# Kernel tuning notes

Hardware: AMD Instinct MI355X
Metric: run time of the kernel (lower is better)

Reference implementation:

```python
import jax, jax.numpy as jnp
import numpy as np

D_MODEL = 1024
HEADS = 16
DEPTH = D_MODEL // HEADS
B, S = 4, 4096
EPS_K = 1e-6  # kernel feature epsilon
EPS_LN = 1e-6


def setup_inputs() -> dict:
    key = jax.random.key(0)
    ks = jax.random.split(key, 8)
    lecun = 1.0 / np.sqrt(D_MODEL)  # LecunNormal stddev
    glorot = np.sqrt(2.0 / (D_MODEL + D_MODEL))  # keras Dense default
    return {
        "q": jax.random.normal(ks[0], (B, S, D_MODEL), jnp.float32),
        "k": jax.random.normal(ks[1], (B, S, D_MODEL), jnp.float32),
        "v": jax.random.normal(ks[2], (B, S, D_MODEL), jnp.float32),
        "mask": jnp.ones((B, S), jnp.float32),
        "wq": jax.random.normal(ks[3], (D_MODEL, D_MODEL), jnp.float32) * lecun,
        "wk": jax.random.normal(ks[4], (D_MODEL, D_MODEL), jnp.float32) * lecun,
        "wv": jax.random.normal(ks[5], (D_MODEL, D_MODEL), jnp.float32) * lecun,
        "ln_gamma": jnp.ones((D_MODEL,), jnp.float32),
        "ln_beta": jnp.zeros((D_MODEL,), jnp.float32),
        "dense_w": jax.random.normal(ks[6], (D_MODEL, D_MODEL), jnp.float32) * glorot,
        "dense_b": jnp.zeros((D_MODEL,), jnp.float32),
    }


def _layernorm(x, g, b):
    m = jnp.mean(x, axis=-1, keepdims=True)
    var = jnp.var(x, axis=-1, keepdims=True)
    return (x - m) * jax.lax.rsqrt(var + EPS_LN) * g + b


def _split_heads(x):
    bsz, sl, _ = x.shape
    return x.reshape(bsz, sl, HEADS, DEPTH).transpose(0, 2, 1, 3)  # [B,H,S,depth]


def reference(q, k, v, mask, wq, wk, wv, ln_gamma, ln_beta, dense_w, dense_b):
    bsz = q.shape[0]
    em = mask[:, None, :, None]  # [B,1,S,1] broadcast over heads/depth
    qh = _split_heads(_layernorm(q @ wq, ln_gamma, ln_beta))
    kh = _split_heads(_layernorm(k @ wk, ln_gamma, ln_beta))
    vh = _split_heads(_layernorm(v @ wv, ln_gamma, ln_beta))
    q_prime = jax.nn.relu(qh) + EPS_K
    k_prime = (jax.nn.relu(kh) + EPS_K) * em
    vh = vh * em
    kv = jnp.einsum('bhnd,bhne->bhde', k_prime, vh)  # [B,H,depth,depth]
    z = 1.0 / (jnp.einsum('bhnd,bhd->bhn', q_prime, k_prime.sum(axis=-2)) + EPS_K)
    att = jnp.einsum('bhnd,bhde,bhn->bhne', q_prime, kv, z)  # [B,H,S,depth]
    # Faithful to original: reshape WITHOUT transposing heads back.
    att = att.reshape(bsz, -1, D_MODEL)  # [B,S,d_model]
    out = att @ dense_w + dense_b
    return _layernorm(out, ln_gamma, ln_beta)
```

## Files before the change

kernel.cpp:

```cpp
#include <hip/hip_runtime.h>
#include <hip/hip_bf16.h>
#include <stdint.h>

#define D_MODEL 1024
#define S_LEN   4096
#define BATCH   4
#define HEADS   16
#define DEPTH   64
#define ROWS    (BATCH*S_LEN)
#define EPS_K_F 1e-6f
#define EPS_LN_F 1e-6f

typedef __attribute__((ext_vector_type(8))) short short8;
typedef __attribute__((ext_vector_type(4))) float f32x4;

__device__ __forceinline__ unsigned short f2bf(float f) {
  union { float f; unsigned u; } x; x.f = f;
  unsigned r = x.u + 0x7FFF + ((x.u >> 16) & 1);
  return (unsigned short)(r >> 16);
}
__device__ __forceinline__ float bf2f(unsigned short b) {
  union { unsigned u; float f; } x; x.u = ((unsigned)b) << 16;
  return x.f;
}
__device__ __forceinline__ void gload16(const void* g, void* l) {
  __builtin_amdgcn_global_load_lds(
      (const __attribute__((address_space(1))) void*)g,
      (__attribute__((address_space(3))) void*)l, 16, 0, 0);
}

__global__ __launch_bounds__(256) void cvt_f32_bf16_k(
    const float* __restrict__ in, unsigned short* __restrict__ out, int n4) {
  int i = blockIdx.x * 256 + threadIdx.x;
  if (i < n4) {
    float4 v = ((const float4*)in)[i];
    ushort4 o;
    o.x = f2bf(v.x); o.y = f2bf(v.y); o.z = f2bf(v.z); o.w = f2bf(v.w);
    ((ushort4*)out)[i] = o;
  }
}

__global__ __launch_bounds__(256) void wtrans_k(
    const float* __restrict__ W, unsigned short* __restrict__ Wt) {
  __shared__ float tile[32][33];
  int n0 = blockIdx.x * 32, k0 = blockIdx.y * 32;
  int tx = threadIdx.x & 31, ty = threadIdx.x >> 5;
  #pragma unroll
  for (int i = 0; i < 32; i += 8)
    tile[ty + i][tx] = W[(size_t)(k0 + ty + i) * D_MODEL + n0 + tx];
  __syncthreads();
  #pragma unroll
  for (int i = 0; i < 32; i += 8)
    Wt[(size_t)(n0 + ty + i) * D_MODEL + k0 + tx] = f2bf(tile[tx][ty + i]);
}

__global__ __launch_bounds__(512, 2) void gemm_bt_k(
    const unsigned short* __restrict__ A,
    const unsigned short* __restrict__ Bt,
    unsigned short* __restrict__ Cb,
    float* __restrict__ psum, float* __restrict__ psq,
    const float* __restrict__ bias,
    int M, int N, int K) {
  __shared__ unsigned short Al[2][256 * 64];
  __shared__ unsigned short Bl[2][256 * 64];
  int t = threadIdx.x;
  int lane = t & 63, wid = t >> 6;
  int wr = wid >> 2, wcn = wid & 3;
  int l15 = lane & 15, lhi = lane >> 4;
  int p = blockIdx.x;
  int cb = (p >> 3) & 3;
  int rb = (p & 7) | ((p >> 5) << 3);
  size_t m0 = (size_t)rb * 256, n0 = (size_t)cb * 256;
  f32x4 acc[8][4] = {};

  const int KT = K >> 6;
  #pragma unroll
  for (int sub = 0; sub < 4; ++sub) {
    int idx = sub * 512 + t;
    int r = idx >> 3, cl = idx & 7;
    int cg = cl ^ (r & 7);
    gload16(A  + (m0 + r) * (size_t)K + cg * 8, &Al[0][idx * 8]);
    gload16(Bt + (n0 + r) * (size_t)K + cg * 8, &Bl[0][idx * 8]);
  }
  asm volatile("s_waitcnt vmcnt(0)" ::: "memory");
  __builtin_amdgcn_s_barrier();
  __builtin_amdgcn_sched_barrier(0);

  for (int kt = 0; kt < KT; ++kt) {
    int cbuf = kt & 1;
    bool pf = (kt + 1) < KT;
    int k0n = (kt + 1) << 6;
    #pragma unroll
    for (int ph = 0; ph < 4; ++ph) {
      const int kk = ph >> 1, mh = ph & 1;
      if (pf && ph == 0) {
        #pragma unroll
        for (int sub = 0; sub < 4; ++sub) {
          int idx = sub * 512 + t;
          int r = idx >> 3, cl = idx & 7;
          int cg = cl ^ (r & 7);
          gload16(A + (m0 + r) * (size_t)K + k0n + cg * 8,
                  &Al[cbuf ^ 1][idx * 8]);
        }
        __builtin_amdgcn_sched_barrier(0);
      }
      if (pf && ph == 1) {
        #pragma unroll
        for (int sub = 0; sub < 4; ++sub) {
          int idx = sub * 512 + t;
          int r = idx >> 3, cl = idx & 7;
          int cg = cl ^ (r & 7);
          gload16(Bt + (n0 + r) * (size_t)K + k0n + cg * 8,
                  &Bl[cbuf ^ 1][idx * 8]);
        }
        __builtin_amdgcn_sched_barrier(0);
      }
      const int cx = (kk * 4 + lhi) ^ (l15 & 7);
      short8 af[4], bfr[4];
      #pragma unroll
      for (int m = 0; m < 4; ++m) {
        int r = wr * 128 + (mh * 4 + m) * 16 + l15;
        af[m] = *(const short8*)&Al[cbuf][r * 64 + cx * 8];
      }
      #pragma unroll
      for (int n = 0; n < 4; ++n) {
        int s = wcn * 64 + n * 16 + l15;
        bfr[n] = *(const short8*)&Bl[cbuf][s * 64 + cx * 8];
      }
      __builtin_amdgcn_s_setprio(1);
      #pragma unroll
      for (int m = 0; m < 4; ++m)
        #pragma unroll
        for (int n = 0; n < 4; ++n)
          acc[mh * 4 + m][n] = __builtin_amdgcn_mfma_f32_16x16x32_bf16(
              af[m], bfr[n], acc[mh * 4 + m][n], 0, 0, 0);
      __builtin_amdgcn_s_setprio(0);
    }
    asm volatile("s_waitcnt vmcnt(0) lgkmcnt(0)" ::: "memory");
    __builtin_amdgcn_s_barrier();
    __builtin_amdgcn_sched_barrier(0);
  }

  if (bias) {
    float bv[4];
    #pragma unroll
    for (int n = 0; n < 4; ++n)
      bv[n] = bias[(int)n0 + wcn * 64 + n * 16 + l15];
    #pragma unroll
    for (int m = 0; m < 8; ++m)
      #pragma unroll
      for (int n = 0; n < 4; ++n)
        #pragma unroll
        for (int j = 0; j < 4; ++j)
          acc[m][n][j] += bv[n];
  }

  int seg = (int)(n0 >> 6) + wcn;
  #pragma unroll
  for (int m = 0; m < 8; ++m) {
    float s[4], s2[4];
    #pragma unroll
    for (int j = 0; j < 4; ++j) {
      float a = 0.f, b = 0.f;
      #pragma unroll
      for (int n = 0; n < 4; ++n) {
        float x = acc[m][n][j];
        a += x; b += x * x;
      }
      s[j] = a; s2[j] = b;
    }
    #pragma unroll
    for (int off = 1; off < 16; off <<= 1) {
      #pragma unroll
      for (int j = 0; j < 4; ++j) {
        s[j]  += __shfl_xor(s[j],  off);
        s2[j] += __shfl_xor(s2[j], off);
      }
    }
    if (l15 == 0) {
      #pragma unroll
      for (int j = 0; j < 4; ++j) {
        int rg = (int)m0 + wr * 128 + m * 16 + lhi * 4 + j;
        psum[rg * 16 + seg] = s[j];
        psq [rg * 16 + seg] = s2[j];
      }
    }
  }

  #pragma unroll
  for (int m = 0; m < 8; ++m)
    #pragma unroll
    for (int j = 0; j < 4; ++j) {
      size_t row = m0 + wr * 128 + m * 16 + lhi * 4 + j;
      #pragma unroll
      for (int n = 0; n < 4; ++n) {
        int col = (int)n0 + wcn * 64 + n * 16 + l15;
        Cb[row * N + col] = f2bf(acc[m][n][j]);
      }
    }
}

__global__ __launch_bounds__(256) void ln_act_k(
    const unsigned short* __restrict__ Cb,
    const float* __restrict__ psum, const float* __restrict__ psq,
    const float* __restrict__ gamma, const float* __restrict__ beta,
    const float* __restrict__ mask,
    unsigned short* __restrict__ out, int mode) {
  int row = blockIdx.x;
  int t = threadIdx.x;
  float s = 0.f, s2 = 0.f;
  #pragma unroll
  for (int i = 0; i < 16; ++i) { s += psum[row * 16 + i]; s2 += psq[row * 16 + i]; }
  float mean = s * (1.f / D_MODEL);
  float var = s2 * (1.f / D_MODEL) - mean * mean;
  float rstd = rsqrtf(var + EPS_LN_F);
  float mk = (mode > 0) ? mask[row] : 1.f;
  ushort4 cv = ((const ushort4*)(Cb + (size_t)row * D_MODEL))[t];
  float4 gv = ((const float4*)gamma)[t];
  float4 bv = ((const float4*)beta)[t];
  float av[4] = {bf2f(cv.x), bf2f(cv.y), bf2f(cv.z), bf2f(cv.w)};
  float g4[4] = {gv.x, gv.y, gv.z, gv.w};
  float b4[4] = {bv.x, bv.y, bv.z, bv.w};
  unsigned short ov[4];
  #pragma unroll
  for (int j = 0; j < 4; ++j) {
    float ln = (av[j] - mean) * rstd * g4[j] + b4[j];
    if (mode == 0)      ln = fmaxf(ln, 0.f) + EPS_K_F;
    else if (mode == 1) ln = (fmaxf(ln, 0.f) + EPS_K_F) * mk;
    else                ln = ln * mk;
    ov[j] = f2bf(ln);
  }
  ushort4 o; o.x = ov[0]; o.y = ov[1]; o.z = ov[2]; o.w = ov[3];
  ((ushort4*)(out + (size_t)row * D_MODEL))[t] = o;
}

__global__ __launch_bounds__(256) void ln_final_k(
    const unsigned short* __restrict__ Cb,
    const float* __restrict__ psum, const float* __restrict__ psq,
    const float* __restrict__ gamma, const float* __restrict__ beta,
    float* __restrict__ out) {
  int row = blockIdx.x;
  int t = threadIdx.x;
  float s = 0.f, s2 = 0.f;
  #pragma unroll
  for (int i = 0; i < 16; ++i) { s += psum[row * 16 + i]; s2 += psq[row * 16 + i]; }
  float mean = s * (1.f / D_MODEL);
  float var = s2 * (1.f / D_MODEL) - mean * mean;
  float rstd = rsqrtf(var + EPS_LN_F);
  ushort4 cv = ((const ushort4*)(Cb + (size_t)row * D_MODEL))[t];
  float4 gv = ((const float4*)gamma)[t];
  float4 bv = ((const float4*)beta)[t];
  float4 w;
  w.x = (bf2f(cv.x) - mean) * rstd * gv.x + bv.x;
  w.y = (bf2f(cv.y) - mean) * rstd * gv.y + bv.y;
  w.z = (bf2f(cv.z) - mean) * rstd * gv.z + bv.z;
  w.w = (bf2f(cv.w) - mean) * rstd * gv.w + bv.w;
  ((float4*)(out + (size_t)row * D_MODEL))[t] = w;
}

__global__ __launch_bounds__(256) void kv_mfma_k(
    const unsigned short* __restrict__ Kp, const unsigned short* __restrict__ Vp,
    float* __restrict__ part, float* __restrict__ kspart) {
  __shared__ unsigned short Kl[4096];
  __shared__ unsigned short Vl[4096];
  int bh = blockIdx.y, chunk = blockIdx.x;
  int b_ = bh >> 4, h = bh & 15;
  int t = threadIdx.x, lane = t & 63, w = t >> 6;
  int l15 = lane & 15, g = lane >> 4;

  int sn = t >> 2, sd16 = t & 3;
  int sc = sd16 ^ ((sn >> 3) & 3);
  size_t goff = (size_t)sn * D_MODEL + h * DEPTH + sd16 * 16;
  int ldst = sn * 64 + sc * 16;

  short8 ones;
  #pragma unroll
  for (int i = 0; i < 8; ++i) ones[i] = (short)0x3F80;

  f32x4 acc[4] = {};
  f32x4 ks = {};

  int baseA = ((w ^ g) << 4) + l15;
  int baseB0 = ((0 ^ g) << 4) + l15;
  int baseB1 = ((1 ^ g) << 4) + l15;
  int baseB2 = ((2 ^ g) << 4) + l15;
  int baseB3 = ((3 ^ g) << 4) + l15;

  size_t rowbase = ((size_t)b_ * S_LEN + (size_t)chunk * 512) * D_MODEL;
  for (int tile = 0; tile < 8; ++tile) {
    const unsigned short* kg = Kp + rowbase + (size_t)tile * 64 * D_MODEL + goff;
    const unsigned short* vg = Vp + rowbase + (size_t)tile * 64 * D_MODEL + goff;
    uint4 ra = *(const uint4*)kg;
    uint4 rb = *(const uint4*)(kg + 8);
    uint4 rc = *(const uint4*)vg;
    uint4 rd = *(const uint4*)(vg + 8);
    __syncthreads();
    *(uint4*)&Kl[ldst]     = ra;
    *(uint4*)&Kl[ldst + 8] = rb;
    *(uint4*)&Vl[ldst]     = rc;
    *(uint4*)&Vl[ldst + 8] = rd;
    __syncthreads();
    #pragma unroll
    for (int kk = 0; kk < 2; ++kk) {
      int nb = (kk * 32 + g * 8) * 64;
      short8 af, bf0, bf1, bf2, bf3;
      #pragma unroll
      for (int i = 0; i < 8; ++i) {
        int rowoff = nb + i * 64;
        af[i]  = (short)Kl[rowoff + baseA];
        bf0[i] = (short)Vl[rowoff + baseB0];
        bf1[i] = (short)Vl[rowoff + baseB1];
        bf2[i] = (short)Vl[rowoff + baseB2];
        bf3[i] = (short)Vl[rowoff + baseB3];
      }
      acc[0] = __builtin_amdgcn_mfma_f32_16x16x32_bf16(af, bf0, acc[0], 0, 0, 0);
      acc[1] = __builtin_amdgcn_mfma_f32_16x16x32_bf16(af, bf1, acc[1], 0, 0, 0);
      acc[2] = __builtin_amdgcn_mfma_f32_16x16x32_bf16(af, bf2, acc[2], 0, 0, 0);
      acc[3] = __builtin_amdgcn_mfma_f32_16x16x32_bf16(af, bf3, acc[3], 0, 0, 0);
      ks     = __builtin_amdgcn_mfma_f32_16x16x32_bf16(af, ones, ks, 0, 0, 0);
    }
  }
  float* pp = part + ((size_t)bh * 8 + chunk) * 4096;
  #pragma unroll
  for (int nf = 0; nf < 4; ++nf)
    #pragma unroll
    for (int r = 0; r < 4; ++r)
      pp[(16 * w + 4 * g + r) * 64 + 16 * nf + l15] = acc[nf][r];
  if (l15 == 0) {
    #pragma unroll
    for (int r = 0; r < 4; ++r)
      kspart[((size_t)bh * 8 + chunk) * 64 + 16 * w + 4 * g + r] = ks[r];
  }
}

__global__ __launch_bounds__(256) void kv_reduce_k(
    const float* __restrict__ part, const float* __restrict__ kspart,
    unsigned short* __restrict__ KVT, float* __restrict__ ksum) {
  int bh = blockIdx.x, t = threadIdx.x;
  for (int idx = t; idx < 4096; idx += 256) {
    int d = idx >> 6, e = idx & 63;
    float s = 0.f;
    #pragma unroll
    for (int c = 0; c < 8; ++c)
      s += part[((size_t)bh * 8 + c) * 4096 + d * 64 + e];
    KVT[(size_t)bh * 4096 + e * 64 + d] = f2bf(s);
  }
  if (t < 64) {
    float s = 0.f;
    #pragma unroll
    for (int c = 0; c < 8; ++c) s += kspart[((size_t)bh * 8 + c) * 64 + t];
    ksum[bh * 64 + t] = s;
  }
}

__global__ __launch_bounds__(256) void att_k(
    const unsigned short* __restrict__ Qp, const unsigned short* __restrict__ KVT,
    const float* __restrict__ ksum, unsigned short* __restrict__ att) {
  __shared__ unsigned short Ql[128 * 64];
  __shared__ unsigned short Kl[64 * 64];
  __shared__ float ksl[64];
  __shared__ float zl[128];
  int bh = blockIdx.y;
  int b = bh >> 4, h = bh & 15;
  int r0 = blockIdx.x * 128;
  int t = threadIdx.x, lane = t & 63, wid = t >> 6;
  int l15 = lane & 15, lhi = lane >> 4;
  #pragma unroll
  for (int i = 0; i < 4; ++i) {
    int cid = i * 256 + t;
    int r = cid >> 3, c8 = cid & 7;
    gload16(Qp + ((size_t)(b * S_LEN + r0 + r)) * D_MODEL + h * DEPTH + c8 * 8,
            &Ql[cid * 8]);
  }
  #pragma unroll
  for (int i = 0; i < 2; ++i) {
    int cid = i * 256 + t;
    gload16(KVT + (size_t)bh * 4096 + cid * 8, &Kl[cid * 8]);
  }
  if (t < 64) ksl[t] = ksum[bh * 64 + t];
  asm volatile("s_waitcnt vmcnt(0)" ::: "memory");
  __syncthreads();
  {
    int r = t >> 1, half = t & 1;
    float s = 0.f;
    #pragma unroll
    for (int j = 0; j < 32; ++j)
      s += bf2f(Ql[r * 64 + half * 32 + j]) * ksl[half * 32 + j];
    s += __shfl_xor(s, 1);
    if (half == 0) zl[r] = 1.f / (s + EPS_K_F);
  }
  __syncthreads();
  f32x4 acc[2][4] = {};
  #pragma unroll
  for (int kk = 0; kk < 2; ++kk) {
    short8 af[2], bfr[4];
    #pragma unroll
    for (int m = 0; m < 2; ++m)
      af[m] = *(const short8*)&Ql[(wid * 32 + m * 16 + l15) * 64 + kk * 32 + lhi * 8];
    #pragma unroll
    for (int n = 0; n < 4; ++n)
      bfr[n] = *(const short8*)&Kl[(n * 16 + l15) * 64 + kk * 32 + lhi * 8];
    #pragma unroll
    for (int m = 0; m < 2; ++m)
      #pragma unroll
      for (int n = 0; n < 4; ++n)
        acc[m][n] = __builtin_amdgcn_mfma_f32_16x16x32_bf16(af[m], bfr[n], acc[m][n], 0, 0, 0);
  }
  #pragma unroll
  for (int m = 0; m < 2; ++m)
    #pragma unroll
    for (int j = 0; j < 4; ++j) {
      int rl = wid * 32 + m * 16 + lhi * 4 + j;
      int n = r0 + rl;
      float z = zl[rl];
      #pragma unroll
      for (int nf = 0; nf < 4; ++nf) {
        int ee = nf * 16 + l15;
        size_t orow = (size_t)b * S_LEN + h * 256 + (n >> 4);
        int ocol = (n & 15) * 64 + ee;
        att[orow * D_MODEL + ocol] = f2bf(acc[m][nf][j] * z);
      }
    }
}

extern "C" void kernel_launch(void* const* d_in, const int* in_sizes, int n_in,
                              void* d_out, int out_size, void* d_ws, size_t ws_size,
                              hipStream_t stream) {
  (void)in_sizes; (void)n_in; (void)out_size; (void)ws_size;
  const float* q     = (const float*)d_in[0];
  const float* k     = (const float*)d_in[1];
  const float* v     = (const float*)d_in[2];
  const float* mask  = (const float*)d_in[3];
  const float* wq    = (const float*)d_in[4];
  const float* wk    = (const float*)d_in[5];
  const float* wv    = (const float*)d_in[6];
  const float* gamma = (const float*)d_in[7];
  const float* beta  = (const float*)d_in[8];
  const float* dw    = (const float*)d_in[9];
  const float* db    = (const float*)d_in[10];
  float* out = (float*)d_out;

  char* ws = (char*)d_ws;
  unsigned short* Xb  = (unsigned short*)(ws);
  unsigned short* Qp  = (unsigned short*)(ws + 33554432);
  unsigned short* Kp  = (unsigned short*)(ws + 67108864);
  unsigned short* Vp  = (unsigned short*)(ws + 100663296);
  unsigned short* WqT = (unsigned short*)(ws + 134217728);
  unsigned short* WkT = WqT + 1048576;
  unsigned short* WvT = WkT + 1048576;
  unsigned short* WdT = WvT + 1048576;
  float* part   = (float*)(ws);
  float* kspart = (float*)(ws + 8388608);
  unsigned short* KVT = (unsigned short*)(ws + 142606336);
  float* ksum = (float*)(ws + 143130624);
  float* psum = (float*)(ws + 143654912);
  float* psq  = (float*)(ws + 144703488);
  unsigned short* Cqkv = (unsigned short*)d_out;
  unsigned short* Cd   = Qp;

  dim3 b256(256);
  dim3 b512(512);
  int n4 = ROWS * D_MODEL / 4;
  dim3 cvtg(n4 / 256);
  dim3 wtg(32, 32);
  dim3 gemmg(256);
  dim3 lng(ROWS);

  wtrans_k<<<wtg, b256, 0, stream>>>(wq, WqT);
  wtrans_k<<<wtg, b256, 0, stream>>>(wk, WkT);
  wtrans_k<<<wtg, b256, 0, stream>>>(wv, WvT);
  wtrans_k<<<wtg, b256, 0, stream>>>(dw, WdT);

  cvt_f32_bf16_k<<<cvtg, b256, 0, stream>>>(q, Xb, n4);
  gemm_bt_k<<<gemmg, b512, 0, stream>>>(Xb, WqT, Cqkv, psum, psq, nullptr, ROWS, D_MODEL, D_MODEL);
  ln_act_k<<<lng, b256, 0, stream>>>(Cqkv, psum, psq, gamma, beta, nullptr, Qp, 0);

  cvt_f32_bf16_k<<<cvtg, b256, 0, stream>>>(k, Xb, n4);
  gemm_bt_k<<<gemmg, b512, 0, stream>>>(Xb, WkT, Cqkv, psum, psq, nullptr, ROWS, D_MODEL, D_MODEL);
  ln_act_k<<<lng, b256, 0, stream>>>(Cqkv, psum, psq, gamma, beta, mask, Kp, 1);

  cvt_f32_bf16_k<<<cvtg, b256, 0, stream>>>(v, Xb, n4);
  gemm_bt_k<<<gemmg, b512, 0, stream>>>(Xb, WvT, Cqkv, psum, psq, nullptr, ROWS, D_MODEL, D_MODEL);
  ln_act_k<<<lng, b256, 0, stream>>>(Cqkv, psum, psq, gamma, beta, mask, Vp, 2);

  kv_mfma_k<<<dim3(8, 64), b256, 0, stream>>>(Kp, Vp, part, kspart);
  kv_reduce_k<<<dim3(64), b256, 0, stream>>>(part, kspart, KVT, ksum);
  att_k<<<dim3(32, 64), b256, 0, stream>>>(Qp, KVT, ksum, Xb);

  gemm_bt_k<<<gemmg, b512, 0, stream>>>(Xb, WdT, Cd, psum, psq, db, ROWS, D_MODEL, D_MODEL);
  ln_final_k<<<lng, b256, 0, stream>>>(Cd, psum, psq, gamma, beta, out);
}
```

Before: 362.0 us.

## Use four-stage K=32 LDS pipeline with partial vmcnt waits in GEMM

Replaces the double-buffered K=64 tile loop with a four-slot ring of K=32 tiles, keeping three tiles of global loads in flight ahead of compute. The full vmcnt(0) wait each iteration becomes a counted partial wait, so the next tile can be consumed while later loads are still outstanding. The LDS swizzle is adapted to 32-wide rows, and B fragments are loaded once per iteration instead of once per phase. The cost is one barrier per 32 K elements instead of per 64, and a fixed-count wait scheme that depends on each tile issuing exactly four loads per thread.

```diff
diff --git a/kernel.cpp b/kernel.cpp
--- a/kernel.cpp
+++ b/kernel.cpp
@@ -61,8 +61,8 @@
     float* __restrict__ psum, float* __restrict__ psq,
     const float* __restrict__ bias,
     int M, int N, int K) {
-  __shared__ unsigned short Al[2][256 * 64];
-  __shared__ unsigned short Bl[2][256 * 64];
+  __shared__ unsigned short Al[4][256 * 32];
+  __shared__ unsigned short Bl[4][256 * 32];
   int t = threadIdx.x;
   int lane = t & 63, wid = t >> 6;
   int wr = wid >> 2, wcn = wid & 3;
@@ -73,60 +73,53 @@
   size_t m0 = (size_t)rb * 256, n0 = (size_t)cb * 256;
   f32x4 acc[8][4] = {};
 
-  const int KT = K >> 6;
-  #pragma unroll
-  for (int sub = 0; sub < 4; ++sub) {
-    int idx = sub * 512 + t;
-    int r = idx >> 3, cl = idx & 7;
-    int cg = cl ^ (r & 7);
-    gload16(A  + (m0 + r) * (size_t)K + cg * 8, &Al[0][idx * 8]);
-    gload16(Bt + (n0 + r) * (size_t)K + cg * 8, &Bl[0][idx * 8]);
-  }
-  asm volatile("s_waitcnt vmcnt(0)" ::: "memory");
+  const int KT = K >> 5;
+
+#define STAGE_TILE(tile_) do {                                              \
+    int kof_ = (tile_) << 5; int slot_ = (tile_) & 3;                       \
+    _Pragma("unroll")                                                       \
+    for (int rnd = 0; rnd < 2; ++rnd) {                                     \
+      int idx = rnd * 512 + t; int r_ = idx >> 2, cl_ = idx & 3;            \
+      int cg_ = cl_ ^ ((r_ >> 1) & 3);                                      \
+      gload16(A + (m0 + r_) * (size_t)K + kof_ + cg_ * 8,                   \
+              &Al[slot_][idx * 8]);                                         \
+    }                                                                       \
+    _Pragma("unroll")                                                       \
+    for (int rnd = 0; rnd < 2; ++rnd) {                                     \
+      int idx = rnd * 512 + t; int r_ = idx >> 2, cl_ = idx & 3;            \
+      int cg_ = cl_ ^ ((r_ >> 1) & 3);                                      \
+      gload16(Bt + (n0 + r_) * (size_t)K + kof_ + cg_ * 8,                  \
+              &Bl[slot_][idx * 8]);                                         \
+    }                                                                       \
+  } while (0)
+
+  STAGE_TILE(0);
+  STAGE_TILE(1);
+  STAGE_TILE(2);
+  asm volatile("s_waitcnt vmcnt(8)" ::: "memory");
   __builtin_amdgcn_s_barrier();
   __builtin_amdgcn_sched_barrier(0);
 
   for (int kt = 0; kt < KT; ++kt) {
-    int cbuf = kt & 1;
-    bool pf = (kt + 1) < KT;
-    int k0n = (kt + 1) << 6;
-    #pragma unroll
-    for (int ph = 0; ph < 4; ++ph) {
-      const int kk = ph >> 1, mh = ph & 1;
-      if (pf && ph == 0) {
-        #pragma unroll
-        for (int sub = 0; sub < 4; ++sub) {
-          int idx = sub * 512 + t;
-          int r = idx >> 3, cl = idx & 7;
-          int cg = cl ^ (r & 7);
-          gload16(A + (m0 + r) * (size_t)K + k0n + cg * 8,
-                  &Al[cbuf ^ 1][idx * 8]);
-        }
-        __builtin_amdgcn_sched_barrier(0);
-      }
-      if (pf && ph == 1) {
-        #pragma unroll
-        for (int sub = 0; sub < 4; ++sub) {
-          int idx = sub * 512 + t;
-          int r = idx >> 3, cl = idx & 7;
-          int cg = cl ^ (r & 7);
-          gload16(Bt + (n0 + r) * (size_t)K + k0n + cg * 8,
-                  &Bl[cbuf ^ 1][idx * 8]);
-        }
-        __builtin_amdgcn_sched_barrier(0);
-      }
-      const int cx = (kk * 4 + lhi) ^ (l15 & 7);
-      short8 af[4], bfr[4];
+    int slot = kt & 3;
+    if (kt + 3 < KT) STAGE_TILE(kt + 3);
+    __builtin_amdgcn_sched_barrier(0);
+    short8 bfr[4];
+    #pragma unroll
+    for (int n = 0; n < 4; ++n) {
+      int rr = wcn * 64 + n * 16 + l15;
+      bfr[n] = *(const short8*)&Bl[slot][rr * 32 + ((lhi ^ ((rr >> 1) & 3)) << 3)];
+    }
+    #pragma unroll
+    for (int mh = 0; mh < 2; ++mh) {
+      short8 af[4];
       #pragma unroll
       for (int m = 0; m < 4; ++m) {
-        int r = wr * 128 + (mh * 4 + m) * 16 + l15;
-        af[m] = *(const short8*)&Al[cbuf][r * 64 + cx * 8];
-      }
-      #pragma unroll
-      for (int n = 0; n < 4; ++n) {
-        int s = wcn * 64 + n * 16 + l15;
-        bfr[n] = *(const short8*)&Bl[cbuf][s * 64 + cx * 8];
-      }
+        int rr = wr * 128 + (mh * 4 + m) * 16 + l15;
+        af[m] = *(const short8*)&Al[slot][rr * 32 + ((lhi ^ ((rr >> 1) & 3)) << 3)];
+      }
+      asm volatile("s_waitcnt lgkmcnt(0)" ::: "memory");
+      __builtin_amdgcn_sched_barrier(0);
       __builtin_amdgcn_s_setprio(1);
       #pragma unroll
       for (int m = 0; m < 4; ++m)
@@ -136,10 +129,18 @@
               af[m], bfr[n], acc[mh * 4 + m][n], 0, 0, 0);
       __builtin_amdgcn_s_setprio(0);
     }
-    asm volatile("s_waitcnt vmcnt(0) lgkmcnt(0)" ::: "memory");
-    __builtin_amdgcn_s_barrier();
-    __builtin_amdgcn_sched_barrier(0);
-  }
+    if (kt + 1 < KT) {
+      if (kt + 4 <= KT - 1)
+        asm volatile("s_waitcnt vmcnt(8)" ::: "memory");
+      else if (kt + 3 == KT - 1)
+        asm volatile("s_waitcnt vmcnt(4)" ::: "memory");
+      else
+        asm volatile("s_waitcnt vmcnt(0)" ::: "memory");
+      __builtin_amdgcn_s_barrier();
+      __builtin_amdgcn_sched_barrier(0);
+    }
+  }
+#undef STAGE_TILE
 
   if (bias) {
     float bv[4];
```

Result: slower. 391.3 us (+8.1%).

## Fuse fp32-to-bf16 input conversion into QKV projection GEMM A-tile loading

Applied to the files above, without the earlier changes.

Removes the three separate cvt_f32_bf16 passes over the q/k/v inputs. A new GEMM variant loads fp32 A tiles into registers, converts them to bf16 and writes them into swizzled LDS, overlapping this with compute on the other buffer. The bf16 intermediate round-trip through memory goes away, but the A loads now use register staging instead of direct global-to-LDS loads and read twice the bytes per tile. The shared compute loop is also restructured: B fragments are loaded once per kk, prefetch is issued all at once, and an explicit lgkmcnt wait comes before the MFMAs.

```diff
diff --git a/kernel.cpp b/kernel.cpp
--- a/kernel.cpp
+++ b/kernel.cpp
@@ -29,17 +29,6 @@
       (__attribute__((address_space(3))) void*)l, 16, 0, 0);
 }
 
-__global__ __launch_bounds__(256) void cvt_f32_bf16_k(
-    const float* __restrict__ in, unsigned short* __restrict__ out, int n4) {
-  int i = blockIdx.x * 256 + threadIdx.x;
-  if (i < n4) {
-    float4 v = ((const float4*)in)[i];
-    ushort4 o;
-    o.x = f2bf(v.x); o.y = f2bf(v.y); o.z = f2bf(v.z); o.w = f2bf(v.w);
-    ((ushort4*)out)[i] = o;
-  }
-}
-
 __global__ __launch_bounds__(256) void wtrans_k(
     const float* __restrict__ W, unsigned short* __restrict__ Wt) {
   __shared__ float tile[32][33];
@@ -52,6 +41,174 @@
   #pragma unroll
   for (int i = 0; i < 32; i += 8)
     Wt[(size_t)(n0 + ty + i) * D_MODEL + k0 + tx] = f2bf(tile[tx][ty + i]);
+}
+
+
+#define GEMM_EPILOGUE(HASBIAS)                                               \
+  if (HASBIAS) {                                                             \
+    float bv[4];                                                             \
+    _Pragma("unroll")                                                        \
+    for (int n = 0; n < 4; ++n)                                              \
+      bv[n] = bias[(int)n0 + wcn * 64 + n * 16 + l15];                       \
+    _Pragma("unroll")                                                        \
+    for (int m = 0; m < 8; ++m)                                              \
+      _Pragma("unroll")                                                      \
+      for (int n = 0; n < 4; ++n)                                            \
+        _Pragma("unroll")                                                    \
+        for (int j = 0; j < 4; ++j)                                          \
+          acc[m][n][j] += bv[n];                                             \
+  }                                                                          \
+  int seg = (int)(n0 >> 6) + wcn;                                            \
+  _Pragma("unroll")                                                          \
+  for (int m = 0; m < 8; ++m) {                                              \
+    float s[4], s2[4];                                                       \
+    _Pragma("unroll")                                                        \
+    for (int j = 0; j < 4; ++j) {                                            \
+      float a = 0.f, b = 0.f;                                                \
+      _Pragma("unroll")                                                      \
+      for (int n = 0; n < 4; ++n) { float x = acc[m][n][j]; a += x; b += x*x; } \
+      s[j] = a; s2[j] = b;                                                   \
+    }                                                                        \
+    _Pragma("unroll")                                                        \
+    for (int off = 1; off < 16; off <<= 1) {                                 \
+      _Pragma("unroll")                                                      \
+      for (int j = 0; j < 4; ++j) {                                          \
+        s[j]  += __shfl_xor(s[j],  off);                                     \
+        s2[j] += __shfl_xor(s2[j], off);                                     \
+      }                                                                      \
+    }                                                                        \
+    if (l15 == 0) {                                                          \
+      _Pragma("unroll")                                                      \
+      for (int j = 0; j < 4; ++j) {                                          \
+        int rg = (int)m0 + wr * 128 + m * 16 + lhi * 4 + j;                  \
+        psum[rg * 16 + seg] = s[j];                                          \
+        psq [rg * 16 + seg] = s2[j];                                         \
+      }                                                                      \
+    }                                                                        \
+  }                                                                          \
+  _Pragma("unroll")                                                          \
+  for (int m = 0; m < 8; ++m)                                                \
+    _Pragma("unroll")                                                        \
+    for (int j = 0; j < 4; ++j) {                                            \
+      size_t row = m0 + wr * 128 + m * 16 + lhi * 4 + j;                     \
+      _Pragma("unroll")                                                      \
+      for (int n = 0; n < 4; ++n) {                                          \
+        int col = (int)n0 + wcn * 64 + n * 16 + l15;                         \
+        Cb[row * N + col] = f2bf(acc[m][n][j]);                              \
+      }                                                                      \
+    }
+
+#define GEMM_COMPUTE_TILE(ABUF, BBUF)                                        \
+  _Pragma("unroll")                                                          \
+  for (int kk = 0; kk < 2; ++kk) {                                           \
+    short8 bfr[4];                                                           \
+    _Pragma("unroll")                                                        \
+    for (int n = 0; n < 4; ++n) {                                            \
+      int rr = wcn * 64 + n * 16 + l15;                                      \
+      int cx = (kk * 4 + lhi) ^ (l15 & 7);                                   \
+      bfr[n] = *(const short8*)&(BBUF)[rr * 64 + cx * 8];                    \
+    }                                                                        \
+    _Pragma("unroll")                                                        \
+    for (int mh = 0; mh < 2; ++mh) {                                         \
+      short8 af[4];                                                          \
+      _Pragma("unroll")                                                      \
+      for (int m = 0; m < 4; ++m) {                                          \
+        int rr = wr * 128 + (mh * 4 + m) * 16 + l15;                         \
+        int cx = (kk * 4 + lhi) ^ (l15 & 7);                                 \
+        af[m] = *(const short8*)&(ABUF)[rr * 64 + cx * 8];                   \
+      }                                                                      \
+      asm volatile("s_waitcnt lgkmcnt(0)" ::: "memory");                     \
+      __builtin_amdgcn_sched_barrier(0);                                     \
+      __builtin_amdgcn_s_setprio(1);                                         \
+      _Pragma("unroll")                                                      \
+      for (int m = 0; m < 4; ++m)                                            \
+        _Pragma("unroll")                                                    \
+        for (int n = 0; n < 4; ++n)                                          \
+          acc[mh * 4 + m][n] = __builtin_amdgcn_mfma_f32_16x16x32_bf16(      \
+              af[m], bfr[n], acc[mh * 4 + m][n], 0, 0, 0);                   \
+      __builtin_amdgcn_s_setprio(0);                                         \
+    }                                                                        \
+  }
+
+__global__ __launch_bounds__(512, 2) void gemm_f32a_k(
+    const float* __restrict__ Af,
+    const unsigned short* __restrict__ Bt,
+    unsigned short* __restrict__ Cb,
+    float* __restrict__ psum, float* __restrict__ psq,
+    int M, int N, int K) {
+  __shared__ unsigned short Al[2][256 * 64];
+  __shared__ unsigned short Bl[2][256 * 64];
+  int t = threadIdx.x;
+  int lane = t & 63, wid = t >> 6;
+  int wr = wid >> 2, wcn = wid & 3;
+  int l15 = lane & 15, lhi = lane >> 4;
+  int p = blockIdx.x;
+  int cb = (p >> 3) & 3;
+  int rb = (p & 7) | ((p >> 5) << 3);
+  size_t m0 = (size_t)rb * 256, n0 = (size_t)cb * 256;
+  f32x4 acc[8][4] = {};
+
+  const int KT = K >> 6;
+  int arow = t >> 4;
+  int ac = t & 15;
+  int achunk = ((ac >> 1) ^ (arow & 7));
+  int aldso = achunk * 8 + (ac & 1) * 4;
+  float4 areg[8];
+
+#define LOAD_A(kof_) do {                                                    \
+    _Pragma("unroll")                                                        \
+    for (int j = 0; j < 8; ++j)                                              \
+      areg[j] = *(const float4*)(Af + (m0 + j * 32 + arow) * (size_t)K +     \
+                                 (kof_) + ac * 4);                           \
+  } while (0)
+#define WRITE_A(buf_) do {                                                   \
+    _Pragma("unroll")                                                        \
+    for (int j = 0; j < 8; ++j) {                                            \
+      unsigned lo_ = (unsigned)f2bf(areg[j].x) |                             \
+                     ((unsigned)f2bf(areg[j].y) << 16);                      \
+      unsigned hi_ = (unsigned)f2bf(areg[j].z) |                             \
+                     ((unsigned)f2bf(areg[j].w) << 16);                      \
+      uint2 wv_; wv_.x = lo_; wv_.y = hi_;                                   \
+      *(uint2*)&Al[buf_][(j * 32 + arow) * 64 + aldso] = wv_;                \
+    }                                                                        \
+  } while (0)
+#define STAGE_B(kof_, buf_) do {                                             \
+    _Pragma("unroll")                                                        \
+    for (int sub = 0; sub < 4; ++sub) {                                      \
+      int idx = sub * 512 + t; int r_ = idx >> 3, cl_ = idx & 7;             \
+      int cg_ = cl_ ^ (r_ & 7);                                              \
+      gload16(Bt + (n0 + r_) * (size_t)K + (kof_) + cg_ * 8,                 \
+              &Bl[buf_][idx * 8]);                                           \
+    }                                                                        \
+  } while (0)
+
+  LOAD_A(0);
+  STAGE_B(0, 0);
+  WRITE_A(0);
+  asm volatile("s_waitcnt vmcnt(0) lgkmcnt(0)" ::: "memory");
+  __builtin_amdgcn_s_barrier();
+  __builtin_amdgcn_sched_barrier(0);
+
+  for (int kt = 0; kt < KT; ++kt) {
+    int buf = kt & 1;
+    if (kt + 1 < KT) {
+      int kn = (kt + 1) << 6;
+      LOAD_A(kn);
+      STAGE_B(kn, buf ^ 1);
+    }
+    __builtin_amdgcn_sched_barrier(0);
+    GEMM_COMPUTE_TILE(Al[buf], Bl[buf]);
+    if (kt + 1 < KT) WRITE_A(buf ^ 1);
+    asm volatile("s_waitcnt vmcnt(0) lgkmcnt(0)" ::: "memory");
+    __builtin_amdgcn_s_barrier();
+    __builtin_amdgcn_sched_barrier(0);
+  }
+#undef LOAD_A
+#undef WRITE_A
+#undef STAGE_B
+
+  const float* bias = nullptr;
+  GEMM_EPILOGUE(false)
 }
 
 __global__ __launch_bounds__(512, 2) void gemm_bt_k(
@@ -74,130 +231,41 @@
   f32x4 acc[8][4] = {};
 
   const int KT = K >> 6;
-  #pragma unroll
-  for (int sub = 0; sub < 4; ++sub) {
-    int idx = sub * 512 + t;
-    int r = idx >> 3, cl = idx & 7;
-    int cg = cl ^ (r & 7);
-    gload16(A  + (m0 + r) * (size_t)K + cg * 8, &Al[0][idx * 8]);
-    gload16(Bt + (n0 + r) * (size_t)K + cg * 8, &Bl[0][idx * 8]);
-  }
+
+#define STAGE_AB(kof_, buf_) do {                                            \
+    _Pragma("unroll")                                                        \
+    for (int sub = 0; sub < 4; ++sub) {                                      \
+      int idx = sub * 512 + t; int r_ = idx >> 3, cl_ = idx & 7;             \
+      int cg_ = cl_ ^ (r_ & 7);                                              \
+      gload16(A + (m0 + r_) * (size_t)K + (kof_) + cg_ * 8,                  \
+              &Al[buf_][idx * 8]);                                           \
+    }                                                                        \
+    _Pragma("unroll")                                                        \
+    for (int sub = 0; sub < 4; ++sub) {                                      \
+      int idx = sub * 512 + t; int r_ = idx >> 3, cl_ = idx & 7;             \
+      int cg_ = cl_ ^ (r_ & 7);                                              \
+      gload16(Bt + (n0 + r_) * (size_t)K + (kof_) + cg_ * 8,                 \
+              &Bl[buf_][idx * 8]);                                           \
+    }                                                                        \
+  } while (0)
+
+  STAGE_AB(0, 0);
   asm volatile("s_waitcnt vmcnt(0)" ::: "memory");
   __builtin_amdgcn_s_barrier();
   __builtin_amdgcn_sched_barrier(0);
 
   for (int kt = 0; kt < KT; ++kt) {
-    int cbuf = kt & 1;
-    bool pf = (kt + 1) < KT;
-    int k0n = (kt + 1) << 6;
-    #pragma unroll
-    for (int ph = 0; ph < 4; ++ph) {
-      const int kk = ph >> 1, mh = ph & 1;
-      if (pf && ph == 0) {
-        #pragma unroll
-        for (int sub = 0; sub < 4; ++sub) {
-          int idx = sub * 512 + t;
-          int r = idx >> 3, cl = idx & 7;
-          int cg = cl ^ (r & 7);
-          gload16(A + (m0 + r) * (size_t)K + k0n + cg * 8,
-                  &Al[cbuf ^ 1][idx * 8]);
-        }
-        __builtin_amdgcn_sched_barrier(0);
-      }
-      if (pf && ph == 1) {
-        #pragma unroll
-        for (int sub = 0; sub < 4; ++sub) {
-          int idx = sub * 512 + t;
-          int r = idx >> 3, cl = idx & 7;
-          int cg = cl ^ (r & 7);
-          gload16(Bt + (n0 + r) * (size_t)K + k0n + cg * 8,
-                  &Bl[cbuf ^ 1][idx * 8]);
-        }
-        __builtin_amdgcn_sched_barrier(0);
-      }
-      const int cx = (kk * 4 + lhi) ^ (l15 & 7);
-      short8 af[4], bfr[4];
-      #pragma unroll
-      for (int m = 0; m < 4; ++m) {
-        int r = wr * 128 + (mh * 4 + m) * 16 + l15;
-        af[m] = *(const short8*)&Al[cbuf][r * 64 + cx * 8];
-      }
-      #pragma unroll
-      for (int n = 0; n < 4; ++n) {
-        int s = wcn * 64 + n * 16 + l15;
-        bfr[n] = *(const short8*)&Bl[cbuf][s * 64 + cx * 8];
-      }
-      __builtin_amdgcn_s_setprio(1);
-      #pragma unroll
-      for (int m = 0; m < 4; ++m)
-        #pragma unroll
-        for (int n = 0; n < 4; ++n)
-          acc[mh * 4 + m][n] = __builtin_amdgcn_mfma_f32_16x16x32_bf16(
-              af[m], bfr[n], acc[mh * 4 + m][n], 0, 0, 0);
-      __builtin_amdgcn_s_setprio(0);
-    }
+    int buf = kt & 1;
+    if (kt + 1 < KT) STAGE_AB((kt + 1) << 6, buf ^ 1);
+    __builtin_amdgcn_sched_barrier(0);
+    GEMM_COMPUTE_TILE(Al[buf], Bl[buf]);
     asm volatile("s_waitcnt vmcnt(0) lgkmcnt(0)" ::: "memory");
     __builtin_amdgcn_s_barrier();
     __builtin_amdgcn_sched_barrier(0);
   }
-
-  if (bias) {
-    float bv[4];
-    #pragma unroll
-    for (int n = 0; n < 4; ++n)
-      bv[n] = bias[(int)n0 + wcn * 64 + n * 16 + l15];
-    #pragma unroll
-    for (int m = 0; m < 8; ++m)
-      #pragma unroll
-      for (int n = 0; n < 4; ++n)
-        #pragma unroll
-        for (int j = 0; j < 4; ++j)
-          acc[m][n][j] += bv[n];
-  }
-
-  int seg = (int)(n0 >> 6) + wcn;
-  #pragma unroll
-  for (int m = 0; m < 8; ++m) {
-    float s[4], s2[4];
-    #pragma unroll
-    for (int j = 0; j < 4; ++j) {
-      float a = 0.f, b = 0.f;
-      #pragma unroll
-      for (int n = 0; n < 4; ++n) {
-        float x = acc[m][n][j];
-        a += x; b += x * x;
-      }
-      s[j] = a; s2[j] = b;
-    }
-    #pragma unroll
-    for (int off = 1; off < 16; off <<= 1) {
-      #pragma unroll
-      for (int j = 0; j < 4; ++j) {
-        s[j]  += __shfl_xor(s[j],  off);
-        s2[j] += __shfl_xor(s2[j], off);
-      }
-    }
-    if (l15 == 0) {
-      #pragma unroll
-      for (int j = 0; j < 4; ++j) {
-        int rg = (int)m0 + wr * 128 + m * 16 + lhi * 4 + j;
-        psum[rg * 16 + seg] = s[j];
-        psq [rg * 16 + seg] = s2[j];
-      }
-    }
-  }
-
-  #pragma unroll
-  for (int m = 0; m < 8; ++m)
-    #pragma unroll
-    for (int j = 0; j < 4; ++j) {
-      size_t row = m0 + wr * 128 + m * 16 + lhi * 4 + j;
-      #pragma unroll
-      for (int n = 0; n < 4; ++n) {
-        int col = (int)n0 + wcn * 64 + n * 16 + l15;
-        Cb[row * N + col] = f2bf(acc[m][n][j]);
-      }
-    }
+#undef STAGE_AB
+
+  GEMM_EPILOGUE(bias != nullptr)
 }
 
 __global__ __launch_bounds__(256) void ln_act_k(
@@ -460,8 +528,6 @@
 
   dim3 b256(256);
   dim3 b512(512);
-  int n4 = ROWS * D_MODEL / 4;
-  dim3 cvtg(n4 / 256);
   dim3 wtg(32, 32);
   dim3 gemmg(256);
   dim3 lng(ROWS);
@@ -471,16 +537,13 @@
   wtrans_k<<<wtg, b256, 0, stream>>>(wv, WvT);
   wtrans_k<<<wtg, b256, 0, stream>>>(dw, WdT);
 
-  cvt_f32_bf16_k<<<cvtg, b256, 0, stream>>>(q, Xb, n4);
-  gemm_bt_k<<<gemmg, b512, 0, stream>>>(Xb, WqT, Cqkv, psum, psq, nullptr, ROWS, D_MODEL, D_MODEL);
+  gemm_f32a_k<<<gemmg, b512, 0, stream>>>(q, WqT, Cqkv, psum, psq, ROWS, D_MODEL, D_MODEL);
   ln_act_k<<<lng, b256, 0, stream>>>(Cqkv, psum, psq, gamma, beta, nullptr, Qp, 0);
 
-  cvt_f32_bf16_k<<<cvtg, b256, 0, stream>>>(k, Xb, n4);
-  gemm_bt_k<<<gemmg, b512, 0, stream>>>(Xb, WkT, Cqkv, psum, psq, nullptr, ROWS, D_MODEL, D_MODEL);
+  gemm_f32a_k<<<gemmg, b512, 0, stream>>>(k, WkT, Cqkv, psum, psq, ROWS, D_MODEL, D_MODEL);
   ln_act_k<<<lng, b256, 0, stream>>>(Cqkv, psum, psq, gamma, beta, mask, Kp, 1);
 
-  cvt_f32_bf16_k<<<cvtg, b256, 0, stream>>>(v, Xb, n4);
-  gemm_bt_k<<<gemmg, b512, 0, stream>>>(Xb, WvT, Cqkv, psum, psq, nullptr, ROWS, D_MODEL, D_MODEL);
+  gemm_f32a_k<<<gemmg, b512, 0, stream>>>(v, WvT, Cqkv, psum, psq, ROWS, D_MODEL, D_MODEL);
   ln_act_k<<<lng, b256, 0, stream>>>(Cqkv, psum, psq, gamma, beta, mask, Vp, 2);
 
   kv_mfma_k<<<dim3(8, 64), b256, 0, stream>>>(Kp, Vp, part, kspart);
```

Result: slower. 372.8 us (+3.0%).
